# Optimization experiments

Hardware: AMD Instinct MI355X
Metric: run time of the kernel (lower is better)

The kernel has to match this reference:

```python
import jax, jax.numpy as jnp
import numpy as np

BETA = 0.25  # cfg.vq_commitment


def setup_inputs() -> dict:
    key = jax.random.key(0)
    k1, k2 = jax.random.split(key)
    residual = jax.random.normal(k1, (16, 2048, 512), dtype=jnp.float32)
    emb_weight = jax.random.normal(k2, (1024, 512), dtype=jnp.float32) * 0.02
    return {"residual": residual, "emb_weight": emb_weight}


def reference(residual, emb_weight):
    # Euclidean branch (vq_cosine=False), no factorized projection (rvq_code_dim<=0)
    r = residual                                     # [B, T, D]
    z2 = jnp.sum(r * r, axis=-1, keepdims=True)      # [B, T, 1]
    e2 = jnp.sum(emb_weight * emb_weight, axis=-1)   # [N]
    # dist[b,t,n] = ||r_bt||^2 + ||e_n||^2 - 2 <r_bt, e_n>
    dist = z2 + e2 - 2.0 * jnp.einsum('btd,nd->btn', r, emb_weight)
    idx = jnp.argmin(dist, axis=-1)                  # [B, T] int
    z_q = emb_weight[idx]                            # gather, [B, T, D]
    # straight-through estimator
    z_st = residual + jax.lax.stop_gradient(z_q - residual)
    commit = jnp.mean((jax.lax.stop_gradient(z_q) - residual) ** 2)
    codebook = jnp.mean((z_q - jax.lax.stop_gradient(residual)) ** 2)
    loss = BETA * commit + codebook
    return (z_st, loss, dist, idx)
```

## Files before the change

### kernel.cpp

```cpp
#include <hip/hip_runtime.h>
#include <cfloat>
#include <stdint.h>

#define D       512
#define NCODES  1024
#define MROWS   32768

#define ZST_OFF  0
#define LOSS_OFF 16777216
#define DIST_OFF 16777217ull
#define IDX_OFF  50331649

#define WS_Z2   524288
#define WS_E2   557056
#define WS_LOSS 558080

typedef __attribute__((ext_vector_type(4))) float f32x4;
typedef __attribute__((ext_vector_type(4))) int   i32x4;
typedef __bf16 bf16v8 __attribute__((ext_vector_type(8)));

static __device__ __forceinline__ uint32_t f2bf(float x) {
    uint32_t u = __float_as_uint(x);
    return (u + 0x7fffu + ((u >> 16) & 1u)) >> 16;
}
static __device__ __forceinline__ float bf2f(uint32_t h) {
    return __uint_as_float(h << 16);
}
static __device__ __forceinline__ f32x4 MFMA(bf16v8 a, bf16v8 b, f32x4 c) {
    return __builtin_amdgcn_mfma_f32_16x16x32_bf16(a, b, c, 0, 0, 0);
}

__global__ void prepass_kernel(const float* __restrict__ residual,
                               const float* __restrict__ emb,
                               float* __restrict__ ws,
                               float* __restrict__ out) {
    if (blockIdx.x == 0 && threadIdx.x == 0) ws[WS_LOSS] = 0.0f;
    const int gwave = (int)((blockIdx.x * blockDim.x + threadIdx.x) >> 6);
    const int lane  = threadIdx.x & 63;
    const bool isA  = gwave < MROWS;
    const float* src = isA ? residual + (size_t)gwave * D
                           : emb + (size_t)(gwave - MROWS) * D;
    const float4* vp = (const float4*)src;
    float4 x0 = vp[lane * 2];
    float4 x1 = vp[lane * 2 + 1];
    float xs[8] = {x0.x, x0.y, x0.z, x0.w, x1.x, x1.y, x1.z, x1.w};
    uint32_t hp[4], lp[4];
    float s = 0.f;
#pragma unroll
    for (int i = 0; i < 4; ++i) {
        float a = xs[2 * i], b = xs[2 * i + 1];
        s += a * a + b * b;
        uint32_t h0 = f2bf(a), h1 = f2bf(b);
        uint32_t l0 = f2bf(a - bf2f(h0)), l1 = f2bf(b - bf2f(h1));
        hp[i] = h0 | (h1 << 16);
        lp[i] = l0 | (l1 << 16);
    }
#pragma unroll
    for (int off = 32; off > 0; off >>= 1) s += __shfl_xor(s, off);

    const int kt = lane >> 3, c8 = lane & 7;
    i32x4 hv = {(int)hp[0], (int)hp[1], (int)hp[2], (int)hp[3]};
    i32x4 lv = {(int)lp[0], (int)lp[1], (int)lp[2], (int)lp[3]};
    if (isA) {
        const int bm = gwave >> 7, rl = gwave & 127;
        char* dst = (char*)out + (size_t)bm * 262144 + (size_t)kt * 32768
                  + rl * 128 + ((c8 * 16) ^ ((rl & 7) << 4));
        *(i32x4*)dst = hv;
        *(i32x4*)(dst + 16384) = lv;
        if (lane == 0) ws[WS_Z2 + gwave] = s;
    } else {
        const int n = gwave - MROWS, nt = n >> 8, cl = n & 255;
        char* dst = (char*)ws + (size_t)nt * 524288 + (size_t)kt * 65536
                  + cl * 128 + ((c8 * 16) ^ ((cl & 7) << 4));
        *(i32x4*)dst = hv;
        *(i32x4*)(dst + 32768) = lv;
        if (lane == 0) ws[WS_E2 + n] = s;
    }
}

__launch_bounds__(512, 2)
__global__ void vq_main_kernel(const float* __restrict__ residual,
                               const float* __restrict__ emb,
                               float* __restrict__ ws,
                               float* __restrict__ out) {
    __shared__ __align__(16) char smem[98304];
    const int tid  = threadIdx.x;
    const int wid  = tid >> 6, lane = tid & 63;
    const int ln15 = lane & 15, kg = lane >> 4;
    const int wm   = wid >> 2, wn = wid & 3;
    const int bm   = blockIdx.x;
    const int row0 = bm * 128;

    float z2r[16];
#pragma unroll
    for (int mf = 0; mf < 4; ++mf)
#pragma unroll
        for (int j = 0; j < 4; ++j)
            z2r[mf * 4 + j] = ws[WS_Z2 + row0 + wm * 64 + mf * 16 + kg * 4 + j];

    float runv[16];
    int   runi[16];
#pragma unroll
    for (int li = 0; li < 16; ++li) { runv[li] = FLT_MAX; runi[li] = 0; }

    int aoff[4][2], boff[4][2];
#pragma unroll
    for (int mf = 0; mf < 4; ++mf) {
        const int rA = wm * 64 + mf * 16 + ln15;
#pragma unroll
        for (int ks = 0; ks < 2; ++ks)
            aoff[mf][ks] = rA * 128 + ((ks * 64 + kg * 16) ^ ((rA & 7) << 4));
    }
#pragma unroll
    for (int nf = 0; nf < 4; ++nf) {
        const int cB = wn * 64 + nf * 16 + ln15;
#pragma unroll
        for (int ks = 0; ks < 2; ++ks)
            boff[nf][ks] = 32768 + cB * 128 + ((ks * 64 + kg * 16) ^ ((cB & 7) << 4));
    }

    const char* srcA = (const char*)out + (size_t)bm * 262144;
    const char* srcB = (const char*)ws;

    for (int nt = 0; nt < 4; ++nt) {
        f32x4 acc[4][4];
#pragma unroll
        for (int mf = 0; mf < 4; ++mf)
#pragma unroll
            for (int nf = 0; nf < 4; ++nf) acc[mf][nf] = 0.f;

        for (int kt = 0; kt < 8; ++kt) {
            __syncthreads();
            {
                const char* ga = srcA + (size_t)kt * 32768 + wid * 1024 + lane * 16;
                char* la = smem + wid * 1024;
#pragma unroll
                for (int i = 0; i < 4; ++i)
                    __builtin_amdgcn_global_load_lds((const uint32_t*)(ga + i * 8192),
                                                     (uint32_t*)(la + i * 8192), 16, 0, 0);
                const char* gb = srcB + (size_t)nt * 524288 + (size_t)kt * 65536
                               + wid * 1024 + lane * 16;
                char* lb = smem + 32768 + wid * 1024;
#pragma unroll
                for (int i = 0; i < 8; ++i)
                    __builtin_amdgcn_global_load_lds((const uint32_t*)(gb + i * 8192),
                                                     (uint32_t*)(lb + i * 8192), 16, 0, 0);
            }
            __syncthreads();

#pragma unroll
            for (int ks = 0; ks < 2; ++ks) {
                bf16v8 ah[4], al[4], bh[4], bl[4];
#pragma unroll
                for (int mf = 0; mf < 4; ++mf) {
                    ah[mf] = *(const bf16v8*)(smem + aoff[mf][ks]);
                    al[mf] = *(const bf16v8*)(smem + aoff[mf][ks] + 16384);
                }
#pragma unroll
                for (int nf = 0; nf < 4; ++nf) {
                    bh[nf] = *(const bf16v8*)(smem + boff[nf][ks]);
                    bl[nf] = *(const bf16v8*)(smem + boff[nf][ks] + 32768);
                }
#pragma unroll
                for (int mf = 0; mf < 4; ++mf)
#pragma unroll
                    for (int nf = 0; nf < 4; ++nf) {
                        acc[mf][nf] = MFMA(ah[mf], bh[nf], acc[mf][nf]);
                        acc[mf][nf] = MFMA(ah[mf], bl[nf], acc[mf][nf]);
                        acc[mf][nf] = MFMA(al[mf], bh[nf], acc[mf][nf]);
                    }
            }
        }

        float e2v[4];
#pragma unroll
        for (int nf = 0; nf < 4; ++nf)
            e2v[nf] = ws[WS_E2 + nt * 256 + wn * 64 + nf * 16 + ln15];
#pragma unroll
        for (int mf = 0; mf < 4; ++mf)
#pragma unroll
            for (int nf = 0; nf < 4; ++nf)
#pragma unroll
                for (int j = 0; j < 4; ++j) {
                    const float dv = (z2r[mf * 4 + j] + e2v[nf]) - 2.0f * acc[mf][nf][j];
                    const int grow = row0 + wm * 64 + mf * 16 + kg * 4 + j;
                    const int gcol = nt * 256 + wn * 64 + nf * 16 + ln15;
                    out[DIST_OFF + (size_t)grow * 1024 + gcol] = dv;
                    const int li = mf * 4 + j;
                    if (dv < runv[li]) { runv[li] = dv; runi[li] = gcol; }
                }
    }

#pragma unroll
    for (int off = 1; off < 16; off <<= 1) {
#pragma unroll
        for (int li = 0; li < 16; ++li) {
            const float ov = __shfl_xor(runv[li], off);
            const int   oi = __shfl_xor(runi[li], off);
            if (ov < runv[li] || (ov == runv[li] && oi < runi[li])) {
                runv[li] = ov; runi[li] = oi;
            }
        }
    }

    float* smin = (float*)smem;
    int*   sidx = (int*)(smem + 2048);
    int*   srowcode = (int*)(smem + 4096);
    float* swsum = (float*)(smem + 4608);
    __syncthreads();
    if (ln15 == 0) {
#pragma unroll
        for (int mf = 0; mf < 4; ++mf)
#pragma unroll
            for (int j = 0; j < 4; ++j) {
                const int rl = wm * 64 + mf * 16 + kg * 4 + j;
                smin[rl * 4 + wn] = runv[mf * 4 + j];
                sidx[rl * 4 + wn] = runi[mf * 4 + j];
            }
    }
    __syncthreads();
    if (tid < 128) {
        float bv = smin[tid * 4];
        int   bi = sidx[tid * 4];
#pragma unroll
        for (int c = 1; c < 4; ++c) {
            const float v  = smin[tid * 4 + c];
            const int   ci = sidx[tid * 4 + c];
            if (v < bv || (v == bv && ci < bi)) { bv = v; bi = ci; }
        }
        srowcode[tid] = bi;
        out[IDX_OFF + row0 + tid] = (float)bi;
    }
    __syncthreads();

    float lsum = 0.0f;
    for (int e4 = tid; e4 < 128 * 128; e4 += 512) {
        const int rl = e4 >> 7, dq = e4 & 127;
        const size_t gi = (size_t)(row0 + rl) * D + dq * 4;
        float4 rv = *(const float4*)&residual[gi];
        const int code = srowcode[rl];
        float4 ev = *(const float4*)&emb[(size_t)code * D + dq * 4];
        float4 st;
        const float dx = ev.x - rv.x, dy = ev.y - rv.y;
        const float dz = ev.z - rv.z, dw = ev.w - rv.w;
        st.x = rv.x + dx; st.y = rv.y + dy; st.z = rv.z + dz; st.w = rv.w + dw;
        *(float4*)&out[ZST_OFF + gi] = st;
        lsum += dx * dx + dy * dy + dz * dz + dw * dw;
    }
#pragma unroll
    for (int off = 32; off > 0; off >>= 1) lsum += __shfl_xor(lsum, off);
    if (lane == 0) swsum[wid] = lsum;
    __syncthreads();
    if (tid == 0) {
        float s = 0.0f;
#pragma unroll
        for (int w = 0; w < 8; ++w) s += swsum[w];
        atomicAdd(&ws[WS_LOSS], s);
    }
}

__global__ void finalize_kernel(const float* __restrict__ ws,
                                float* __restrict__ out) {
    out[LOSS_OFF] = 1.25f * ws[WS_LOSS] / 16777216.0f;
}

extern "C" void kernel_launch(void* const* d_in, const int* in_sizes, int n_in,
                              void* d_out, int out_size, void* d_ws, size_t ws_size,
                              hipStream_t stream) {
    const float* residual = (const float*)d_in[0];
    const float* emb      = (const float*)d_in[1];
    float* out = (float*)d_out;
    float* ws  = (float*)d_ws;

    prepass_kernel<<<8448, 256, 0, stream>>>(residual, emb, ws, out);
    vq_main_kernel<<<MROWS / 128, 512, 0, stream>>>(residual, emb, ws, out);
    finalize_kernel<<<1, 1, 0, stream>>>(ws, out);
}
```

Before: 399.1 us.

## Restructure VQ into 2D-tiled GEMM with in-kernel A split and separate argmin pass

Replaces the per-row-block kernel that swept all 1024 codes with a 2D-tiled GEMM grid of 128x128 tiles over 256-thread blocks, ordered by XCD. The residual is now converted to bf16 hi/lo inside the GEMM, so the prepass no longer writes an A image to global memory. Loads are double-buffered in LDS. The argmin and the z_st/loss work move to a separate kernel that re-reads the written distance matrix, which adds about 128 MB of extra reads in exchange for more parallelism and no split-A round trip.

```diff
diff --git a/kernel.cpp b/kernel.cpp
--- a/kernel.cpp
+++ b/kernel.cpp
@@ -11,9 +11,8 @@
 #define DIST_OFF 16777217ull
 #define IDX_OFF  50331649
 
-#define WS_Z2   524288
-#define WS_E2   557056
-#define WS_LOSS 558080
+#define WS_E2F   524288
+#define WS_LOSSF 525312
 
 typedef __attribute__((ext_vector_type(4))) float f32x4;
 typedef __attribute__((ext_vector_type(4))) int   i32x4;
@@ -30,216 +29,244 @@
     return __builtin_amdgcn_mfma_f32_16x16x32_bf16(a, b, c, 0, 0, 0);
 }
 
-__global__ void prepass_kernel(const float* __restrict__ residual,
-                               const float* __restrict__ emb,
-                               float* __restrict__ ws,
-                               float* __restrict__ out) {
-    if (blockIdx.x == 0 && threadIdx.x == 0) ws[WS_LOSS] = 0.0f;
-    const int gwave = (int)((blockIdx.x * blockDim.x + threadIdx.x) >> 6);
-    const int lane  = threadIdx.x & 63;
-    const bool isA  = gwave < MROWS;
-    const float* src = isA ? residual + (size_t)gwave * D
-                           : emb + (size_t)(gwave - MROWS) * D;
-    const float4* vp = (const float4*)src;
-    float4 x0 = vp[lane * 2];
-    float4 x1 = vp[lane * 2 + 1];
-    float xs[8] = {x0.x, x0.y, x0.z, x0.w, x1.x, x1.y, x1.z, x1.w};
-    uint32_t hp[4], lp[4];
-    float s = 0.f;
+__global__ void split_e_kernel(const float* __restrict__ emb,
+                               char* __restrict__ wsb,
+                               float* __restrict__ wsf) {
+    if (blockIdx.x == 0 && threadIdx.x == 0) wsf[WS_LOSSF] = 0.0f;
+    const int u    = blockIdx.x * 256 + threadIdx.x;
+    const int row  = u >> 5;
+    const int ks   = (u >> 1) & 15;
+    const int half = u & 1;
+    const float* p = emb + (size_t)row * D + ks * 32 + half * 16;
+    float xs[16];
 #pragma unroll
     for (int i = 0; i < 4; ++i) {
-        float a = xs[2 * i], b = xs[2 * i + 1];
-        s += a * a + b * b;
-        uint32_t h0 = f2bf(a), h1 = f2bf(b);
-        uint32_t l0 = f2bf(a - bf2f(h0)), l1 = f2bf(b - bf2f(h1));
-        hp[i] = h0 | (h1 << 16);
-        lp[i] = l0 | (l1 << 16);
-    }
+        const float4 v = ((const float4*)p)[i];
+        xs[4*i] = v.x; xs[4*i+1] = v.y; xs[4*i+2] = v.z; xs[4*i+3] = v.w;
+    }
+    uint32_t hw[8], lw[8];
+#pragma unroll
+    for (int i = 0; i < 8; ++i) {
+        const float a = xs[2*i], b = xs[2*i+1];
+        const uint32_t h0 = f2bf(a), h1 = f2bf(b);
+        const uint32_t l0 = f2bf(a - bf2f(h0)), l1 = f2bf(b - bf2f(h1));
+        hw[i] = h0 | (h1 << 16);
+        lw[i] = l0 | (l1 << 16);
+    }
+    const int nblk = row >> 7, col = row & 127;
+    char* base = wsb + (size_t)nblk * 262144 + (size_t)ks * 16384 + col * 128;
+    const int sw = col & 7;
+    *(i32x4*)(base + 16 * ((half*2    ) ^ sw)) = i32x4{(int)hw[0],(int)hw[1],(int)hw[2],(int)hw[3]};
+    *(i32x4*)(base + 16 * ((half*2 + 1) ^ sw)) = i32x4{(int)hw[4],(int)hw[5],(int)hw[6],(int)hw[7]};
+    *(i32x4*)(base + 16 * ((4 + half*2    ) ^ sw)) = i32x4{(int)lw[0],(int)lw[1],(int)lw[2],(int)lw[3]};
+    *(i32x4*)(base + 16 * ((4 + half*2 + 1) ^ sw)) = i32x4{(int)lw[4],(int)lw[5],(int)lw[6],(int)lw[7]};
+}
+
+__global__ void e2_kernel(const float* __restrict__ emb,
+                          float* __restrict__ wsf) {
+    const int gw   = (int)((blockIdx.x * blockDim.x + threadIdx.x) >> 6);
+    const int lane = threadIdx.x & 63;
+    const float4* v = (const float4*)(emb + (size_t)gw * D);
+    const float4 a = v[lane * 2];
+    const float4 b = v[lane * 2 + 1];
+    float s = a.x*a.x + a.y*a.y + a.z*a.z + a.w*a.w
+            + b.x*b.x + b.y*b.y + b.z*b.z + b.w*b.w;
 #pragma unroll
     for (int off = 32; off > 0; off >>= 1) s += __shfl_xor(s, off);
-
-    const int kt = lane >> 3, c8 = lane & 7;
-    i32x4 hv = {(int)hp[0], (int)hp[1], (int)hp[2], (int)hp[3]};
-    i32x4 lv = {(int)lp[0], (int)lp[1], (int)lp[2], (int)lp[3]};
-    if (isA) {
-        const int bm = gwave >> 7, rl = gwave & 127;
-        char* dst = (char*)out + (size_t)bm * 262144 + (size_t)kt * 32768
-                  + rl * 128 + ((c8 * 16) ^ ((rl & 7) << 4));
-        *(i32x4*)dst = hv;
-        *(i32x4*)(dst + 16384) = lv;
-        if (lane == 0) ws[WS_Z2 + gwave] = s;
-    } else {
-        const int n = gwave - MROWS, nt = n >> 8, cl = n & 255;
-        char* dst = (char*)ws + (size_t)nt * 524288 + (size_t)kt * 65536
-                  + cl * 128 + ((c8 * 16) ^ ((cl & 7) << 4));
-        *(i32x4*)dst = hv;
-        *(i32x4*)(dst + 32768) = lv;
-        if (lane == 0) ws[WS_E2 + n] = s;
-    }
-}
-
-__launch_bounds__(512, 2)
-__global__ void vq_main_kernel(const float* __restrict__ residual,
-                               const float* __restrict__ emb,
-                               float* __restrict__ ws,
-                               float* __restrict__ out) {
-    __shared__ __align__(16) char smem[98304];
-    const int tid  = threadIdx.x;
-    const int wid  = tid >> 6, lane = tid & 63;
+    if (lane == 0) wsf[WS_E2F + gw] = s;
+}
+
+__launch_bounds__(256, 2)
+__global__ void gemm_kernel(const float* __restrict__ residual,
+                            const char* __restrict__ wsb,
+                            const float* __restrict__ wsf,
+                            float* __restrict__ out) {
+    __shared__ __align__(16) char smem[66048];
+    float* z2s = (float*)(smem + 65536);
+
+    const int t    = threadIdx.x;
+    const int lane = t & 63, wid = t >> 6;
     const int ln15 = lane & 15, kg = lane >> 4;
-    const int wm   = wid >> 2, wn = wid & 3;
-    const int bm   = blockIdx.x;
-    const int row0 = bm * 128;
-
-    float z2r[16];
-#pragma unroll
-    for (int mf = 0; mf < 4; ++mf)
-#pragma unroll
-        for (int j = 0; j < 4; ++j)
-            z2r[mf * 4 + j] = ws[WS_Z2 + row0 + wm * 64 + mf * 16 + kg * 4 + j];
-
-    float runv[16];
-    int   runi[16];
-#pragma unroll
-    for (int li = 0; li < 16; ++li) { runv[li] = FLT_MAX; runi[li] = 0; }
-
-    int aoff[4][2], boff[4][2];
+    const int wm   = wid >> 1, wn = wid & 1;
+
+    const int bid  = blockIdx.x;
+    const int xcd  = bid & 7, j = bid >> 3;
+    const int mblk = xcd * 32 + (j >> 3);
+    const int nblk = j & 7;
+    const int row0 = mblk * 128;
+    const int n0   = nblk * 128;
+
+    const int arow = t >> 1, ahalf = t & 1;
+    const float* asrc = residual + (size_t)(row0 + arow) * D + ahalf * 16;
+    const int asw = arow & 7;
+    char* awbase = nullptr;
+
+    int aoffh[4], aoffl[4], boffh[4], boffl[4];
 #pragma unroll
     for (int mf = 0; mf < 4; ++mf) {
         const int rA = wm * 64 + mf * 16 + ln15;
-#pragma unroll
-        for (int ks = 0; ks < 2; ++ks)
-            aoff[mf][ks] = rA * 128 + ((ks * 64 + kg * 16) ^ ((rA & 7) << 4));
+        aoffh[mf] = rA * 128 + 16 * ((    kg) ^ (rA & 7));
+        aoffl[mf] = rA * 128 + 16 * ((4 + kg) ^ (rA & 7));
     }
 #pragma unroll
     for (int nf = 0; nf < 4; ++nf) {
         const int cB = wn * 64 + nf * 16 + ln15;
-#pragma unroll
-        for (int ks = 0; ks < 2; ++ks)
-            boff[nf][ks] = 32768 + cB * 128 + ((ks * 64 + kg * 16) ^ ((cB & 7) << 4));
-    }
-
-    const char* srcA = (const char*)out + (size_t)bm * 262144;
-    const char* srcB = (const char*)ws;
-
-    for (int nt = 0; nt < 4; ++nt) {
-        f32x4 acc[4][4];
+        boffh[nf] = 16384 + cB * 128 + 16 * ((    kg) ^ (cB & 7));
+        boffl[nf] = 16384 + cB * 128 + 16 * ((4 + kg) ^ (cB & 7));
+    }
+
+    const char* Bimg = wsb + (size_t)nblk * 262144;
+
+    float z2p = 0.0f;
+
+    auto LOAD_A = [&](int s, f32x4 na[4]) {
+        const float* p = asrc + s * 32;
+#pragma unroll
+        for (int i = 0; i < 4; ++i) na[i] = *(const f32x4*)(p + 4 * i);
+    };
+    auto WRITE_A = [&](char* buf, const f32x4 na[4]) {
+        float xs[16];
+#pragma unroll
+        for (int i = 0; i < 4; ++i) {
+            xs[4*i] = na[i][0]; xs[4*i+1] = na[i][1];
+            xs[4*i+2] = na[i][2]; xs[4*i+3] = na[i][3];
+        }
+        uint32_t hw[8], lw[8];
+#pragma unroll
+        for (int i = 0; i < 8; ++i) {
+            const float a = xs[2*i], b = xs[2*i+1];
+            z2p += a * a + b * b;
+            const uint32_t h0 = f2bf(a), h1 = f2bf(b);
+            const uint32_t l0 = f2bf(a - bf2f(h0)), l1 = f2bf(b - bf2f(h1));
+            hw[i] = h0 | (h1 << 16);
+            lw[i] = l0 | (l1 << 16);
+        }
+        char* base = buf + arow * 128;
+        *(i32x4*)(base + 16 * ((ahalf*2    ) ^ asw)) = i32x4{(int)hw[0],(int)hw[1],(int)hw[2],(int)hw[3]};
+        *(i32x4*)(base + 16 * ((ahalf*2 + 1) ^ asw)) = i32x4{(int)hw[4],(int)hw[5],(int)hw[6],(int)hw[7]};
+        *(i32x4*)(base + 16 * ((4 + ahalf*2    ) ^ asw)) = i32x4{(int)lw[0],(int)lw[1],(int)lw[2],(int)lw[3]};
+        *(i32x4*)(base + 16 * ((4 + ahalf*2 + 1) ^ asw)) = i32x4{(int)lw[4],(int)lw[5],(int)lw[6],(int)lw[7]};
+    };
+    auto STAGE_B = [&](int s, char* buf) {
+        const char* gb = Bimg + (size_t)s * 16384 + wid * 4096 + lane * 16;
+        char* lb = buf + 16384 + wid * 4096;
+#pragma unroll
+        for (int i = 0; i < 4; ++i)
+            __builtin_amdgcn_global_load_lds((const uint32_t*)(gb + i * 1024),
+                                             (uint32_t*)(lb + i * 1024), 16, 0, 0);
+    };
+
+    f32x4 acc[4][4];
+#pragma unroll
+    for (int mf = 0; mf < 4; ++mf)
+#pragma unroll
+        for (int nf = 0; nf < 4; ++nf) acc[mf][nf] = 0.f;
+
+    {
+        f32x4 na[4];
+        LOAD_A(0, na);
+        STAGE_B(0, smem);
+        WRITE_A(smem, na);
+    }
+
+    for (int s = 0; s < 16; ++s) {
+        __syncthreads();
+        char* nbuf = smem + ((s + 1) & 1) * 32768;
+        f32x4 na[4];
+        if (s < 15) {
+            LOAD_A(s + 1, na);
+            STAGE_B(s + 1, nbuf);
+        }
+        const char* buf = smem + (s & 1) * 32768;
+
+        bf16v8 ah[4], al[4], bh[4], bl[4];
+#pragma unroll
+        for (int mf = 0; mf < 4; ++mf) {
+            ah[mf] = *(const bf16v8*)(buf + aoffh[mf]);
+            al[mf] = *(const bf16v8*)(buf + aoffl[mf]);
+        }
+#pragma unroll
+        for (int nf = 0; nf < 4; ++nf) {
+            bh[nf] = *(const bf16v8*)(buf + boffh[nf]);
+            bl[nf] = *(const bf16v8*)(buf + boffl[nf]);
+        }
 #pragma unroll
         for (int mf = 0; mf < 4; ++mf)
 #pragma unroll
-            for (int nf = 0; nf < 4; ++nf) acc[mf][nf] = 0.f;
-
-        for (int kt = 0; kt < 8; ++kt) {
-            __syncthreads();
-            {
-                const char* ga = srcA + (size_t)kt * 32768 + wid * 1024 + lane * 16;
-                char* la = smem + wid * 1024;
-#pragma unroll
-                for (int i = 0; i < 4; ++i)
-                    __builtin_amdgcn_global_load_lds((const uint32_t*)(ga + i * 8192),
-                                                     (uint32_t*)(la + i * 8192), 16, 0, 0);
-                const char* gb = srcB + (size_t)nt * 524288 + (size_t)kt * 65536
-                               + wid * 1024 + lane * 16;
-                char* lb = smem + 32768 + wid * 1024;
-#pragma unroll
-                for (int i = 0; i < 8; ++i)
-                    __builtin_amdgcn_global_load_lds((const uint32_t*)(gb + i * 8192),
-                                                     (uint32_t*)(lb + i * 8192), 16, 0, 0);
+            for (int nf = 0; nf < 4; ++nf) {
+                acc[mf][nf] = MFMA(ah[mf], bh[nf], acc[mf][nf]);
+                acc[mf][nf] = MFMA(ah[mf], bl[nf], acc[mf][nf]);
+                acc[mf][nf] = MFMA(al[mf], bh[nf], acc[mf][nf]);
             }
-            __syncthreads();
-
-#pragma unroll
-            for (int ks = 0; ks < 2; ++ks) {
-                bf16v8 ah[4], al[4], bh[4], bl[4];
-#pragma unroll
-                for (int mf = 0; mf < 4; ++mf) {
-                    ah[mf] = *(const bf16v8*)(smem + aoff[mf][ks]);
-                    al[mf] = *(const bf16v8*)(smem + aoff[mf][ks] + 16384);
-                }
-#pragma unroll
-                for (int nf = 0; nf < 4; ++nf) {
-                    bh[nf] = *(const bf16v8*)(smem + boff[nf][ks]);
-                    bl[nf] = *(const bf16v8*)(smem + boff[nf][ks] + 32768);
-                }
-#pragma unroll
-                for (int mf = 0; mf < 4; ++mf)
-#pragma unroll
-                    for (int nf = 0; nf < 4; ++nf) {
-                        acc[mf][nf] = MFMA(ah[mf], bh[nf], acc[mf][nf]);
-                        acc[mf][nf] = MFMA(ah[mf], bl[nf], acc[mf][nf]);
-                        acc[mf][nf] = MFMA(al[mf], bh[nf], acc[mf][nf]);
-                    }
+
+        if (s < 15) WRITE_A(nbuf, na);
+    }
+
+    __syncthreads();
+    {
+        const float o = __shfl_xor(z2p, 1);
+        if (ahalf == 0) z2s[arow] = z2p + o;
+    }
+    __syncthreads();
+
+    float e2v[4];
+#pragma unroll
+    for (int nf = 0; nf < 4; ++nf)
+        e2v[nf] = wsf[WS_E2F + n0 + wn * 64 + nf * 16 + ln15];
+#pragma unroll
+    for (int mf = 0; mf < 4; ++mf)
+#pragma unroll
+        for (int j4 = 0; j4 < 4; ++j4) {
+            const int rl = wm * 64 + mf * 16 + kg * 4 + j4;
+            const float z2 = z2s[rl];
+            const size_t rbase = DIST_OFF + (size_t)(row0 + rl) * 1024;
+#pragma unroll
+            for (int nf = 0; nf < 4; ++nf) {
+                const int gcol = n0 + wn * 64 + nf * 16 + ln15;
+                out[rbase + gcol] = (z2 + e2v[nf]) - 2.0f * acc[mf][nf][j4];
             }
         }
-
-        float e2v[4];
-#pragma unroll
-        for (int nf = 0; nf < 4; ++nf)
-            e2v[nf] = ws[WS_E2 + nt * 256 + wn * 64 + nf * 16 + ln15];
-#pragma unroll
-        for (int mf = 0; mf < 4; ++mf)
-#pragma unroll
-            for (int nf = 0; nf < 4; ++nf)
-#pragma unroll
-                for (int j = 0; j < 4; ++j) {
-                    const float dv = (z2r[mf * 4 + j] + e2v[nf]) - 2.0f * acc[mf][nf][j];
-                    const int grow = row0 + wm * 64 + mf * 16 + kg * 4 + j;
-                    const int gcol = nt * 256 + wn * 64 + nf * 16 + ln15;
-                    out[DIST_OFF + (size_t)grow * 1024 + gcol] = dv;
-                    const int li = mf * 4 + j;
-                    if (dv < runv[li]) { runv[li] = dv; runi[li] = gcol; }
-                }
-    }
-
-#pragma unroll
-    for (int off = 1; off < 16; off <<= 1) {
-#pragma unroll
-        for (int li = 0; li < 16; ++li) {
-            const float ov = __shfl_xor(runv[li], off);
-            const int   oi = __shfl_xor(runi[li], off);
-            if (ov < runv[li] || (ov == runv[li] && oi < runi[li])) {
-                runv[li] = ov; runi[li] = oi;
-            }
-        }
-    }
-
-    float* smin = (float*)smem;
-    int*   sidx = (int*)(smem + 2048);
-    int*   srowcode = (int*)(smem + 4096);
-    float* swsum = (float*)(smem + 4608);
+}
+
+__global__ void argzst_kernel(const float* __restrict__ residual,
+                              const float* __restrict__ emb,
+                              float* __restrict__ wsf,
+                              float* __restrict__ out) {
+    __shared__ int   srow[64];
+    __shared__ float swsum[4];
+    const int t = threadIdx.x, lane = t & 63, w = t >> 6;
+    const int row0 = blockIdx.x * 64;
+
+    for (int rr = 0; rr < 16; ++rr) {
+        const int row = row0 + w * 16 + rr;
+        const float* dr = out + DIST_OFF + (size_t)row * 1024;
+        float lv = FLT_MAX; int li = 0;
+#pragma unroll
+        for (int c = 0; c < 16; ++c) {
+            const int col = c * 64 + lane;
+            const float v = dr[col];
+            if (v < lv) { lv = v; li = col; }
+        }
+#pragma unroll
+        for (int off = 32; off > 0; off >>= 1) {
+            const float ov = __shfl_xor(lv, off);
+            const int   oi = __shfl_xor(li, off);
+            if (ov < lv || (ov == lv && oi < li)) { lv = ov; li = oi; }
+        }
+        if (lane == 0) {
+            srow[w * 16 + rr] = li;
+            out[IDX_OFF + row] = (float)li;
+        }
+    }
     __syncthreads();
-    if (ln15 == 0) {
-#pragma unroll
-        for (int mf = 0; mf < 4; ++mf)
-#pragma unroll
-            for (int j = 0; j < 4; ++j) {
-                const int rl = wm * 64 + mf * 16 + kg * 4 + j;
-                smin[rl * 4 + wn] = runv[mf * 4 + j];
-                sidx[rl * 4 + wn] = runi[mf * 4 + j];
-            }
-    }
-    __syncthreads();
-    if (tid < 128) {
-        float bv = smin[tid * 4];
-        int   bi = sidx[tid * 4];
-#pragma unroll
-        for (int c = 1; c < 4; ++c) {
-            const float v  = smin[tid * 4 + c];
-            const int   ci = sidx[tid * 4 + c];
-            if (v < bv || (v == bv && ci < bi)) { bv = v; bi = ci; }
-        }
-        srowcode[tid] = bi;
-        out[IDX_OFF + row0 + tid] = (float)bi;
-    }
-    __syncthreads();
 
     float lsum = 0.0f;
-    for (int e4 = tid; e4 < 128 * 128; e4 += 512) {
+    for (int e4 = t; e4 < 64 * 128; e4 += 256) {
         const int rl = e4 >> 7, dq = e4 & 127;
         const size_t gi = (size_t)(row0 + rl) * D + dq * 4;
-        float4 rv = *(const float4*)&residual[gi];
-        const int code = srowcode[rl];
-        float4 ev = *(const float4*)&emb[(size_t)code * D + dq * 4];
+        const float4 rv = *(const float4*)&residual[gi];
+        const int code = srow[rl];
+        const float4 ev = *(const float4*)&emb[(size_t)code * D + dq * 4];
         float4 st;
         const float dx = ev.x - rv.x, dy = ev.y - rv.y;
         const float dz = ev.z - rv.z, dw = ev.w - rv.w;
@@ -249,19 +276,19 @@
     }
 #pragma unroll
     for (int off = 32; off > 0; off >>= 1) lsum += __shfl_xor(lsum, off);
-    if (lane == 0) swsum[wid] = lsum;
+    if (lane == 0) swsum[w] = lsum;
     __syncthreads();
-    if (tid == 0) {
+    if (t == 0) {
         float s = 0.0f;
 #pragma unroll
-        for (int w = 0; w < 8; ++w) s += swsum[w];
-        atomicAdd(&ws[WS_LOSS], s);
-    }
-}
-
-__global__ void finalize_kernel(const float* __restrict__ ws,
+        for (int ww = 0; ww < 4; ++ww) s += swsum[ww];
+        atomicAdd(&wsf[WS_LOSSF], s);
+    }
+}
+
+__global__ void finalize_kernel(const float* __restrict__ wsf,
                                 float* __restrict__ out) {
-    out[LOSS_OFF] = 1.25f * ws[WS_LOSS] / 16777216.0f;
+    out[LOSS_OFF] = 1.25f * wsf[WS_LOSSF] / 16777216.0f;
 }
 
 extern "C" void kernel_launch(void* const* d_in, const int* in_sizes, int n_in,
@@ -270,9 +297,12 @@
     const float* residual = (const float*)d_in[0];
     const float* emb      = (const float*)d_in[1];
     float* out = (float*)d_out;
-    float* ws  = (float*)d_ws;
-
-    prepass_kernel<<<8448, 256, 0, stream>>>(residual, emb, ws, out);
-    vq_main_kernel<<<MROWS / 128, 512, 0, stream>>>(residual, emb, ws, out);
-    finalize_kernel<<<1, 1, 0, stream>>>(ws, out);
-}
+    char*  wsb = (char*)d_ws;
+    float* wsf = (float*)d_ws;
+
+    split_e_kernel<<<128, 256, 0, stream>>>(emb, wsb, wsf);
+    e2_kernel<<<256, 256, 0, stream>>>(emb, wsf);
+    gemm_kernel<<<2048, 256, 0, stream>>>(residual, wsb, wsf, out);
+    argzst_kernel<<<512, 256, 0, stream>>>(residual, emb, wsf, out);
+    finalize_kernel<<<1, 1, 0, stream>>>(wsf, out);
+}
```

Result: slower. 407.6 us (+2.1%).
